# Optimization experiments

Hardware: AMD Instinct MI355X
Metric: run time of the kernel (lower is better)

Reference implementation:

```python
import jax, jax.numpy as jnp
import numpy as np

EPS = 1e-4   # synsin-style z clamp in world_to_view
BIG = 1e10   # z-buffer init


def _xy_grid(h, w):
    xs = jnp.linspace(-1.0, 1.0, w)
    ys = jnp.linspace(-1.0, 1.0, h)
    gy, gx = jnp.meshgrid(ys, xs, indexing='ij')
    return jnp.stack([gx.ravel(), gy.ravel()], 0)  # [2, h*w], NDC pixel rays


def _view_to_world(depth, K_inv, RTinv, xy):
    # depth [B,1,N]; homogeneous coords rows = (x*d, y*d, d, 1)
    proj = jnp.concatenate([xy[None] * depth, depth, jnp.ones_like(depth)], axis=1)  # [B,4,N]
    cam = jnp.einsum('bij,bjn->bin', K_inv, proj)
    return jnp.einsum('bij,bjn->bin', RTinv, cam)  # [B,4,N]


def _world_to_view(world, K, RT):
    cam2 = jnp.einsum('bij,bjn->bin', RT, world)
    xy_proj = jnp.einsum('bij,bjn->bin', K, cam2)
    z = xy_proj[:, 2:3]
    mask = jnp.abs(z) < EPS
    zs = jnp.where(mask, EPS, z)
    sampler = jnp.concatenate([xy_proj[:, 0:2] / zs, z], axis=1)  # [B,3,N]
    return jnp.where(mask, -10.0, sampler)


def _splat_one(sampler, feats, h, w):
    # sampler [3,N] (x,y in NDC, z depth); feats [C,N]. Nearest-pixel z-buffer splat.
    x, y, z = sampler[0], sampler[1], sampler[2]
    n = x.shape[0]
    px = jnp.round((x + 1.0) * 0.5 * (w - 1)).astype(jnp.int32)
    py = jnp.round((y + 1.0) * 0.5 * (h - 1)).astype(jnp.int32)
    valid = (px >= 0) & (px < w) & (py >= 0) & (py < h) & (z > EPS)
    idx = jnp.where(valid, py * w + px, h * w)  # invalid -> dump bucket h*w
    zv = jnp.where(valid, z, BIG)
    zbuf = jnp.full(h * w + 1, BIG, feats.dtype).at[idx].min(zv)
    pid = jnp.where(valid & (zv <= zbuf[idx]), jnp.arange(n, dtype=jnp.int32), n)
    win = jnp.full(h * w + 1, n, jnp.int32).at[idx].min(pid)[: h * w]  # winning point per pixel
    fpad = jnp.concatenate([feats, jnp.zeros((feats.shape[0], 1), feats.dtype)], axis=1)
    out = fpad[:, win].reshape(feats.shape[0], h, w)
    zb = zbuf[: h * w]
    depth = jnp.where(zb < BIG, zb, 0.0).reshape(1, h, w)
    return out, depth


def _project(depths, colors, feats, K, src_RTs, src_RTinvs, dst_RTs, dst_RTinvs):
    B, V, _, Hc, Wc = depths.shape
    _, _, C, Hf, Wf = feats.shape
    sh, sw = Hf / Hc, Wf / Wc
    scale = jnp.array([sw, sh, 1.0, 1.0], depths.dtype)[None, :, None]
    sK = K * scale
    sKinv = jnp.linalg.inv(sK)

    colors_r = jax.image.resize(colors.reshape(B * V, 3, Hc, Wc), (B * V, 3, Hf, Wf),
                                method='linear', antialias=True)
    depths_r = jax.image.resize(depths.reshape(B * V, 1, Hc, Wc), (B * V, 1, Hf, Wf),
                                method='nearest')
    feats_f = feats.reshape(B, V, C, Hf * Wf)
    colors_f = colors_r.reshape(B, V, 3, Hf * Wf)
    depths_f = depths_r.reshape(B, V, 1, Hf * Wf)

    xy = _xy_grid(Hf, Wf)
    dstRT = dst_RTs[:, 0]  # num_outputs == 1
    splat = jax.vmap(lambda s, f: _splat_one(s, f, Hf, Wf))

    results, warped, pdepths = [], [], []
    for i in range(V):  # small fixed number of source views
        world = _view_to_world(depths_f[:, i], sKinv, src_RTinvs[:, i], xy)
        sampler = _world_to_view(world, sK, dstRT)            # [B,3,N]
        src = jnp.concatenate([feats_f[:, i], colors_f[:, i] * 0.5 + 0.5], axis=1)  # [B,C+3,N]
        res, dep = splat(sampler, src)                        # [B,C+3,Hf,Wf], [B,1,Hf,Wf]
        results.append(res[:, :C])
        warped.append(res[:, C:])
        pdepths.append(dep)

    prj_fs = jnp.stack(results, 0)      # [V,B,C,Hf,Wf]
    warped = jnp.stack(warped, 0)       # [V,B,3,Hf,Wf]
    prj_depths = jnp.stack(pdepths, 0)  # [V,B,1,Hf,Wf]
    # forward() permutes prj_fs / prj_depths to [B,V,...]; warped stays [V,B,...]
    return prj_fs.transpose(1, 0, 2, 3, 4), warped, prj_depths.transpose(1, 0, 2, 3, 4)


def setup_inputs() -> dict:
    key = jax.random.key(0)
    k1, k2, k3 = jax.random.split(key, 3)
    B, V, Hc, Wc = 2, 2, 512, 512
    Hf, Wf, C = 256, 256, 64

    depths = jax.random.uniform(k1, (B, V, 1, Hc, Wc), jnp.float32, 1.0, 5.0)
    colors = jax.random.uniform(k2, (B, V, 3, Hc, Wc), jnp.float32, -1.0, 1.0)
    feats = jax.random.normal(k3, (B, V, C, Hf, Wf), jnp.float32)

    K = np.eye(4, dtype=np.float32)  # NDC intrinsic (fx=fy=1, cx=cy=0)
    th = 0.1
    R = np.array([[np.cos(th), 0, np.sin(th), 0.2],
                  [0, 1, 0, 0.0],
                  [-np.sin(th), 0, np.cos(th), 0.1],
                  [0, 0, 0, 1]], dtype=np.float32)
    src_RT = np.eye(4, dtype=np.float32)

    Kb = jnp.asarray(np.tile(K[None], (B, 1, 1)))
    src_RTs = jnp.asarray(np.tile(src_RT[None, None], (B, V, 1, 1)))
    src_RTinvs = src_RTs  # identity
    dst_RTs = jnp.asarray(np.tile(R[None, None], (B, 1, 1, 1)))
    dst_RTinvs = jnp.asarray(np.tile(np.linalg.inv(R)[None, None], (B, 1, 1, 1)))

    return {"depths": depths, "colors": colors, "feats": feats, "K": Kb,
            "src_RTs": src_RTs, "src_RTinvs": src_RTinvs,
            "dst_RTs": dst_RTs, "dst_RTinvs": dst_RTinvs}


def reference(depths, colors, feats, K, src_RTs, src_RTinvs, dst_RTs, dst_RTinvs):
    return _project(depths, colors, feats, K, src_RTs, src_RTinvs, dst_RTs, dst_RTinvs)
```

## Files before the change

kernel.cpp:

```cpp
#include <hip/hip_runtime.h>
#include <stdint.h>

#pragma clang fp contract(off)

namespace {
constexpr int B_ = 2, V_ = 2, HC = 512, WC = 512, HF = 256, WF = 256, CF = 64;
constexpr int NPIX = HF * WF;
constexpr float EPSF = 1e-4f;
constexpr float BIGF = 1e10f;
constexpr int NPT = B_ * V_ * NPIX;
constexpr int NBLK_PT = NPT / 256;
constexpr size_t WS_BASE = (size_t)NPT * 8 + (size_t)B_ * V_ * 3 * NPIX * 4 + 256;
constexpr size_t TF_BYTES = (size_t)NPT * CF * 4;
}

__device__ __forceinline__ float dot4f(const float* __restrict__ r,
                                       float v0, float v1, float v2, float v3) {
  float t = r[0] * v0;
  t = t + r[1] * v1;
  t = t + r[2] * v2;
  t = t + r[3] * v3;
  return t;
}

__global__ void prep_k(const float* __restrict__ K,
                       const float* __restrict__ colors,
                       float* __restrict__ colr,
                       float* __restrict__ mats,
                       unsigned long long* __restrict__ zwin) {
  int g = blockIdx.x * blockDim.x + threadIdx.x;

  if (g < NPT) zwin[g] = ~0ULL;

  if (g < B_) {
    int b = g;
    const float rowscale[4] = {0.5f, 0.5f, 1.0f, 1.0f};
    float sK[16];
    for (int i = 0; i < 4; ++i)
      for (int j = 0; j < 4; ++j)
        sK[i*4+j] = K[b*16 + i*4 + j] * rowscale[i];
    double m[16];
    for (int i = 0; i < 16; ++i) m[i] = (double)sK[i];
    double inv[16];
    inv[0]  =  m[5]*m[10]*m[15] - m[5]*m[11]*m[14] - m[9]*m[6]*m[15] + m[9]*m[7]*m[14] + m[13]*m[6]*m[11] - m[13]*m[7]*m[10];
    inv[4]  = -m[4]*m[10]*m[15] + m[4]*m[11]*m[14] + m[8]*m[6]*m[15] - m[8]*m[7]*m[14] - m[12]*m[6]*m[11] + m[12]*m[7]*m[10];
    inv[8]  =  m[4]*m[9]*m[15]  - m[4]*m[11]*m[13] - m[8]*m[5]*m[15] + m[8]*m[7]*m[13] + m[12]*m[5]*m[11] - m[12]*m[7]*m[9];
    inv[12] = -m[4]*m[9]*m[14]  + m[4]*m[10]*m[13] + m[8]*m[5]*m[14] - m[8]*m[6]*m[13] - m[12]*m[5]*m[10] + m[12]*m[6]*m[9];
    inv[1]  = -m[1]*m[10]*m[15] + m[1]*m[11]*m[14] + m[9]*m[2]*m[15] - m[9]*m[3]*m[14] - m[13]*m[2]*m[11] + m[13]*m[3]*m[10];
    inv[5]  =  m[0]*m[10]*m[15] - m[0]*m[11]*m[14] - m[8]*m[2]*m[15] + m[8]*m[3]*m[14] + m[12]*m[2]*m[11] - m[12]*m[3]*m[10];
    inv[9]  = -m[0]*m[9]*m[15]  + m[0]*m[11]*m[13] + m[8]*m[1]*m[15] - m[8]*m[3]*m[13] - m[12]*m[1]*m[11] + m[12]*m[3]*m[9];
    inv[13] =  m[0]*m[9]*m[14]  - m[0]*m[10]*m[13] - m[8]*m[1]*m[14] + m[8]*m[2]*m[13] + m[12]*m[1]*m[10] - m[12]*m[2]*m[9];
    inv[2]  =  m[1]*m[6]*m[15]  - m[1]*m[7]*m[14]  - m[5]*m[2]*m[15] + m[5]*m[3]*m[14] + m[13]*m[2]*m[7]  - m[13]*m[3]*m[6];
    inv[6]  = -m[0]*m[6]*m[15]  + m[0]*m[7]*m[14]  + m[4]*m[2]*m[15] - m[4]*m[3]*m[14] - m[12]*m[2]*m[7]  + m[12]*m[3]*m[6];
    inv[10] =  m[0]*m[5]*m[15]  - m[0]*m[7]*m[13]  - m[4]*m[1]*m[15] + m[4]*m[3]*m[13] + m[12]*m[1]*m[7]  - m[12]*m[3]*m[5];
    inv[14] = -m[0]*m[5]*m[14]  + m[0]*m[6]*m[13]  + m[4]*m[1]*m[14] - m[4]*m[2]*m[13] - m[12]*m[1]*m[6]  + m[12]*m[2]*m[5];
    inv[3]  = -m[1]*m[6]*m[11]  + m[1]*m[7]*m[10]  + m[5]*m[2]*m[11] - m[5]*m[3]*m[10] - m[9]*m[2]*m[7]   + m[9]*m[3]*m[6];
    inv[7]  =  m[0]*m[6]*m[11]  - m[0]*m[7]*m[10]  - m[4]*m[2]*m[11] + m[4]*m[3]*m[10] + m[8]*m[2]*m[7]   - m[8]*m[3]*m[6];
    inv[11] = -m[0]*m[5]*m[11]  + m[0]*m[7]*m[9]   + m[4]*m[1]*m[11] - m[4]*m[3]*m[9]  - m[8]*m[1]*m[7]   + m[8]*m[3]*m[5];
    inv[15] =  m[0]*m[5]*m[10]  - m[0]*m[6]*m[9]   - m[4]*m[1]*m[10] + m[4]*m[2]*m[9]  + m[8]*m[1]*m[6]   - m[8]*m[2]*m[5];
    double det = m[0]*inv[0] + m[1]*inv[4] + m[2]*inv[8] + m[3]*inv[12];
    double idet = 1.0 / det;
    for (int i = 0; i < 16; ++i) {
      mats[b*32 + i]      = sK[i];
      mats[b*32 + 16 + i] = (float)(inv[i] * idet);
    }
  }

  if (g >= B_ * V_ * 3 * NPIX) return;
  int pc  = g >> 16;
  int pix = g & (NPIX - 1);
  int y = pix >> 8, x = pix & (WF - 1);
  const float* src = colors + (size_t)pc * HC * WC;
  const float W37 = (float)(3.0 / 7.0), W17 = (float)(1.0 / 7.0);
  float wy[4] = {0.125f, 0.375f, 0.375f, 0.125f};
  float wx[4] = {0.125f, 0.375f, 0.375f, 0.125f};
  if (y == 0)      { wy[0] = 0.f; wy[1] = W37; wy[2] = W37; wy[3] = W17; }
  if (y == HF - 1) { wy[0] = W17; wy[1] = W37; wy[2] = W37; wy[3] = 0.f; }
  if (x == 0)      { wx[0] = 0.f; wx[1] = W37; wx[2] = W37; wx[3] = W17; }
  if (x == WF - 1) { wx[0] = W17; wx[1] = W37; wx[2] = W37; wx[3] = 0.f; }
  int jy0 = 2 * y - 1, jx0 = 2 * x - 1;
  float acc = 0.f;
  #pragma unroll
  for (int ty = 0; ty < 4; ++ty) {
    if (wy[ty] == 0.f) continue;
    int jy = jy0 + ty;
    float rs = 0.f;
    #pragma unroll
    for (int tx = 0; tx < 4; ++tx) {
      if (wx[tx] == 0.f) continue;
      rs = rs + wx[tx] * src[(size_t)jy * WC + (jx0 + tx)];
    }
    acc = acc + wy[ty] * rs;
  }
  colr[g] = acc;
}

__global__ void transp_k(const float* __restrict__ feats,
                         float* __restrict__ tf) {
  __shared__ float lds[CF][65];
  int bid = blockIdx.x;
  int bv = bid >> 10;
  int pix0 = (bid & 1023) << 6;
  int t = threadIdx.x;
  int sub = t >> 4;
  int l16 = t & 15;
  const float* fb = feats + (size_t)bv * CF * NPIX;
  #pragma unroll
  for (int pass = 0; pass < 4; ++pass) {
    int ch = pass * 16 + sub;
    const float4 v = *(const float4*)(fb + (size_t)ch * NPIX + pix0 + 4 * l16);
    lds[ch][4*l16+0] = v.x; lds[ch][4*l16+1] = v.y;
    lds[ch][4*l16+2] = v.z; lds[ch][4*l16+3] = v.w;
  }
  __syncthreads();
  float* tb = tf + ((size_t)bv * NPIX + pix0) * CF;
  #pragma unroll
  for (int pass = 0; pass < 4; ++pass) {
    int p = pass * 16 + sub;
    float4 w;
    w.x = lds[4*l16+0][p]; w.y = lds[4*l16+1][p];
    w.z = lds[4*l16+2][p]; w.w = lds[4*l16+3][p];
    *(float4*)(tb + (size_t)p * CF + 4 * l16) = w;
  }
}

__global__ void splat_k(const float* __restrict__ depths,
                        const float* __restrict__ mats,
                        const float* __restrict__ srcRTinv,
                        const float* __restrict__ dstRT,
                        unsigned long long* __restrict__ zwin) {
  int g = blockIdx.x * blockDim.x + threadIdx.x;
  if (g >= NPT) return;
  int bv = g >> 16;
  int n  = g & (NPIX - 1);
  int b  = bv / V_;
  int y = n >> 8, x = n & (WF - 1);
  float d = depths[(size_t)bv * HC * WC + (size_t)(2 * y + 1) * WC + (2 * x + 1)];
  const float step32 = 2.0f / 255.0f;
  float xf = (float)x * step32 - 1.0f;
  float yf = (float)y * step32 - 1.0f;
  float pr0 = xf * d, pr1 = yf * d, pr2 = d, pr3 = 1.0f;
  const float* sK  = mats + b * 32;
  const float* sKi = mats + b * 32 + 16;
  const float* Rs  = srcRTinv + (size_t)bv * 16;
  const float* Rd  = dstRT + (size_t)b * 16;
  float a0 = dot4f(sKi + 0,  pr0, pr1, pr2, pr3);
  float a1 = dot4f(sKi + 4,  pr0, pr1, pr2, pr3);
  float a2 = dot4f(sKi + 8,  pr0, pr1, pr2, pr3);
  float a3 = dot4f(sKi + 12, pr0, pr1, pr2, pr3);
  float w0 = dot4f(Rs + 0,  a0, a1, a2, a3);
  float w1 = dot4f(Rs + 4,  a0, a1, a2, a3);
  float w2 = dot4f(Rs + 8,  a0, a1, a2, a3);
  float w3 = dot4f(Rs + 12, a0, a1, a2, a3);
  float c0 = dot4f(Rd + 0,  w0, w1, w2, w3);
  float c1 = dot4f(Rd + 4,  w0, w1, w2, w3);
  float c2 = dot4f(Rd + 8,  w0, w1, w2, w3);
  float c3 = dot4f(Rd + 12, w0, w1, w2, w3);
  float p0 = dot4f(sK + 0, c0, c1, c2, c3);
  float p1 = dot4f(sK + 4, c0, c1, c2, c3);
  float p2 = dot4f(sK + 8, c0, c1, c2, c3);
  if (!(p2 > EPSF)) return;
  float sx = p0 / p2, sy = p1 / p2;
  float pxf = rintf(((sx + 1.0f) * 0.5f) * 255.0f);
  float pyf = rintf(((sy + 1.0f) * 0.5f) * 255.0f);
  if (!(pxf >= 0.0f && pxf <= 255.0f && pyf >= 0.0f && pyf <= 255.0f)) return;
  int idx = (int)pyf * WF + (int)pxf;
  unsigned zbits = __float_as_uint(p2);
  unsigned long long key = ((unsigned long long)zbits << 32) | (unsigned)n;
  atomicMin(&zwin[(size_t)bv * NPIX + idx], key);
}

__global__ void gatherT_k(const unsigned long long* __restrict__ zwin,
                          const float* __restrict__ tf,
                          const float* __restrict__ colr,
                          float* __restrict__ out0,
                          float* __restrict__ out1,
                          float* __restrict__ out2) {
  int g = blockIdx.x * 256 + threadIdx.x;
  int bv = g >> 16;
  int pix = g & (NPIX - 1);
  unsigned long long key = zwin[g];
  bool hit = (key != ~0ULL);
  int n = (int)(key & 0xffffffffULL);
  float4 f[16];
  if (hit) {
    const float4* src = (const float4*)(tf + ((size_t)bv * NPIX + n) * CF);
    #pragma unroll
    for (int i = 0; i < 16; ++i) f[i] = src[i];
  } else {
    #pragma unroll
    for (int i = 0; i < 16; ++i) f[i] = make_float4(0.f, 0.f, 0.f, 0.f);
  }
  float* o0 = out0 + (size_t)bv * CF * NPIX + pix;
  const float* fs = (const float*)f;
  #pragma unroll
  for (int c = 0; c < CF; ++c)
    __builtin_nontemporal_store(fs[c], &o0[(size_t)c * NPIX]);

  int b = bv >> 1, v = bv & 1;
  const float* cb = colr + (size_t)bv * 3 * NPIX;
  float* o1 = out1 + (size_t)(v * B_ + b) * 3 * NPIX + pix;
  if (hit) {
    float z = __uint_as_float((unsigned)(key >> 32));
    __builtin_nontemporal_store((z < BIGF) ? z : 0.0f, &out2[g]);
    #pragma unroll
    for (int ch = 0; ch < 3; ++ch)
      __builtin_nontemporal_store(cb[(size_t)ch * NPIX + n] * 0.5f + 0.5f,
                                  &o1[(size_t)ch * NPIX]);
  } else {
    __builtin_nontemporal_store(0.0f, &out2[g]);
    #pragma unroll
    for (int ch = 0; ch < 3; ++ch)
      __builtin_nontemporal_store(0.0f, &o1[(size_t)ch * NPIX]);
  }
}

__global__ void gather_k(const unsigned long long* __restrict__ zwin,
                         const float* __restrict__ feats,
                         const float* __restrict__ colr,
                         float* __restrict__ out0,
                         float* __restrict__ out1,
                         float* __restrict__ out2) {
  int bid = blockIdx.x;
  int grp = bid >> 10;
  int g   = (bid & (NBLK_PT - 1)) * 256 + threadIdx.x;
  int bv  = g >> 16;
  int pix = g & (NPIX - 1);
  unsigned long long key = zwin[g];
  bool hit = (key != ~0ULL);
  int n = (int)(key & 0xffffffffULL);

  if (grp < 4) {
    int c0 = grp * 16;
    const float* fb = feats + (size_t)bv * CF * NPIX + (size_t)c0 * NPIX;
    float* o0 = out0 + (size_t)bv * CF * NPIX + (size_t)c0 * NPIX + pix;
    if (hit) {
      #pragma unroll
      for (int c = 0; c < 16; ++c)
        __builtin_nontemporal_store(fb[(size_t)c * NPIX + n], &o0[(size_t)c * NPIX]);
    } else {
      #pragma unroll
      for (int c = 0; c < 16; ++c)
        __builtin_nontemporal_store(0.0f, &o0[(size_t)c * NPIX]);
    }
  } else {
    int b = bv >> 1, v = bv & 1;
    const float* cb = colr + (size_t)bv * 3 * NPIX;
    float* o1 = out1 + (size_t)(v * B_ + b) * 3 * NPIX + pix;
    if (hit) {
      float z = __uint_as_float((unsigned)(key >> 32));
      __builtin_nontemporal_store((z < BIGF) ? z : 0.0f, &out2[g]);
      #pragma unroll
      for (int ch = 0; ch < 3; ++ch)
        __builtin_nontemporal_store(cb[(size_t)ch * NPIX + n] * 0.5f + 0.5f,
                                    &o1[(size_t)ch * NPIX]);
    } else {
      __builtin_nontemporal_store(0.0f, &out2[g]);
      #pragma unroll
      for (int ch = 0; ch < 3; ++ch)
        __builtin_nontemporal_store(0.0f, &o1[(size_t)ch * NPIX]);
    }
  }
}

extern "C" void kernel_launch(void* const* d_in, const int* in_sizes, int n_in,
                              void* d_out, int out_size, void* d_ws, size_t ws_size,
                              hipStream_t stream) {
  const float* depths     = (const float*)d_in[0];
  const float* colors     = (const float*)d_in[1];
  const float* feats      = (const float*)d_in[2];
  const float* K          = (const float*)d_in[3];
  const float* src_RTinvs = (const float*)d_in[5];
  const float* dst_RTs    = (const float*)d_in[6];

  float* out0 = (float*)d_out;
  float* out1 = out0 + (size_t)B_ * V_ * CF * NPIX;
  float* out2 = out1 + (size_t)V_ * B_ * 3 * NPIX;

  unsigned long long* zwin = (unsigned long long*)d_ws;
  float* colr = (float*)(zwin + NPT);
  float* mats = colr + (size_t)B_ * V_ * 3 * NPIX;
  float* tf   = (float*)((char*)d_ws + WS_BASE);

  const bool use_tf = (ws_size >= WS_BASE + TF_BYTES);

  prep_k<<<(B_ * V_ * 3 * NPIX) / 256, 256, 0, stream>>>(K, colors, colr, mats, zwin);
  if (use_tf)
    transp_k<<<B_ * V_ * (NPIX / 64), 256, 0, stream>>>(feats, tf);
  splat_k<<<NBLK_PT, 256, 0, stream>>>(depths, mats, src_RTinvs, dst_RTs, zwin);
  if (use_tf)
    gatherT_k<<<NBLK_PT, 256, 0, stream>>>(zwin, tf, colr, out0, out1, out2);
  else
    gather_k<<<5 * NBLK_PT, 256, 0, stream>>>(zwin, feats, colr, out0, out1, out2);
}
```

Before: 184.7 us.

## Fuse feature transpose into prep kernel and split gather across channel groups

Moves the feature transpose into the prep kernel as extra blocks, which removes one kernel launch and lets transpose and colour resize run concurrently. Also splits the transposed gather kernel into five block groups: four each handle 16 feature channels and one handles colour and depth. This gives five times more blocks with fewer registers per thread, for more memory parallelism, at the cost of rereading zwin five times. The prep kernel now allocates LDS in every block, including the resize blocks that never use it, which may lower occupancy.

New measurement: 180.5 us. 2.3% less time.

```diff
diff --git a/kernel.cpp b/kernel.cpp
--- a/kernel.cpp
+++ b/kernel.cpp
@@ -10,6 +10,8 @@
 constexpr float BIGF = 1e10f;
 constexpr int NPT = B_ * V_ * NPIX;
 constexpr int NBLK_PT = NPT / 256;
+constexpr int RESIZE_BLKS = (B_ * V_ * 3 * NPIX) / 256;
+constexpr int TRANSP_BLKS = B_ * V_ * (NPIX / 64);
 constexpr size_t WS_BASE = (size_t)NPT * 8 + (size_t)B_ * V_ * 3 * NPIX * 4 + 256;
 constexpr size_t TF_BYTES = (size_t)NPT * CF * 4;
 }
@@ -25,10 +27,43 @@
 
 __global__ void prep_k(const float* __restrict__ K,
                        const float* __restrict__ colors,
+                       const float* __restrict__ feats,
                        float* __restrict__ colr,
                        float* __restrict__ mats,
-                       unsigned long long* __restrict__ zwin) {
-  int g = blockIdx.x * blockDim.x + threadIdx.x;
+                       unsigned long long* __restrict__ zwin,
+                       float* __restrict__ tf) {
+  __shared__ float lds[CF][65];
+  int bid = blockIdx.x;
+  int nT = (int)gridDim.x - RESIZE_BLKS;
+  int t = threadIdx.x;
+
+  if (bid < nT) {
+    int bv = bid >> 10;
+    int pix0 = (bid & 1023) << 6;
+    int sub = t >> 4;
+    int l16 = t & 15;
+    const float* fb = feats + (size_t)bv * CF * NPIX;
+    #pragma unroll
+    for (int pass = 0; pass < 4; ++pass) {
+      int ch = pass * 16 + sub;
+      const float4 v = *(const float4*)(fb + (size_t)ch * NPIX + pix0 + 4 * l16);
+      lds[ch][4*l16+0] = v.x; lds[ch][4*l16+1] = v.y;
+      lds[ch][4*l16+2] = v.z; lds[ch][4*l16+3] = v.w;
+    }
+    __syncthreads();
+    float* tb = tf + ((size_t)bv * NPIX + pix0) * CF;
+    #pragma unroll
+    for (int pass = 0; pass < 4; ++pass) {
+      int p = pass * 16 + sub;
+      float4 w;
+      w.x = lds[4*l16+0][p]; w.y = lds[4*l16+1][p];
+      w.z = lds[4*l16+2][p]; w.w = lds[4*l16+3][p];
+      *(float4*)(tb + (size_t)p * CF + 4 * l16) = w;
+    }
+    return;
+  }
+
+  int g = (bid - nT) * 256 + t;
 
   if (g < NPT) zwin[g] = ~0ULL;
 
@@ -66,7 +101,6 @@
     }
   }
 
-  if (g >= B_ * V_ * 3 * NPIX) return;
   int pc  = g >> 16;
   int pix = g & (NPIX - 1);
   int y = pix >> 8, x = pix & (WF - 1);
@@ -93,35 +127,6 @@
     acc = acc + wy[ty] * rs;
   }
   colr[g] = acc;
-}
-
-__global__ void transp_k(const float* __restrict__ feats,
-                         float* __restrict__ tf) {
-  __shared__ float lds[CF][65];
-  int bid = blockIdx.x;
-  int bv = bid >> 10;
-  int pix0 = (bid & 1023) << 6;
-  int t = threadIdx.x;
-  int sub = t >> 4;
-  int l16 = t & 15;
-  const float* fb = feats + (size_t)bv * CF * NPIX;
-  #pragma unroll
-  for (int pass = 0; pass < 4; ++pass) {
-    int ch = pass * 16 + sub;
-    const float4 v = *(const float4*)(fb + (size_t)ch * NPIX + pix0 + 4 * l16);
-    lds[ch][4*l16+0] = v.x; lds[ch][4*l16+1] = v.y;
-    lds[ch][4*l16+2] = v.z; lds[ch][4*l16+3] = v.w;
-  }
-  __syncthreads();
-  float* tb = tf + ((size_t)bv * NPIX + pix0) * CF;
-  #pragma unroll
-  for (int pass = 0; pass < 4; ++pass) {
-    int p = pass * 16 + sub;
-    float4 w;
-    w.x = lds[4*l16+0][p]; w.y = lds[4*l16+1][p];
-    w.z = lds[4*l16+2][p]; w.w = lds[4*l16+3][p];
-    *(float4*)(tb + (size_t)p * CF + 4 * l16) = w;
-  }
 }
 
 __global__ void splat_k(const float* __restrict__ depths,
@@ -176,42 +181,48 @@
                           float* __restrict__ out0,
                           float* __restrict__ out1,
                           float* __restrict__ out2) {
-  int g = blockIdx.x * 256 + threadIdx.x;
-  int bv = g >> 16;
+  int bid = blockIdx.x;
+  int grp = bid >> 10;
+  int g   = (bid & (NBLK_PT - 1)) * 256 + threadIdx.x;
+  int bv  = g >> 16;
   int pix = g & (NPIX - 1);
   unsigned long long key = zwin[g];
   bool hit = (key != ~0ULL);
   int n = (int)(key & 0xffffffffULL);
-  float4 f[16];
-  if (hit) {
-    const float4* src = (const float4*)(tf + ((size_t)bv * NPIX + n) * CF);
+
+  if (grp < 4) {
+    float4 f[4];
+    if (hit) {
+      const float4* src =
+          (const float4*)(tf + ((size_t)bv * NPIX + n) * CF + grp * 16);
+      #pragma unroll
+      for (int i = 0; i < 4; ++i) f[i] = src[i];
+    } else {
+      #pragma unroll
+      for (int i = 0; i < 4; ++i) f[i] = make_float4(0.f, 0.f, 0.f, 0.f);
+    }
+    float* o0 = out0 + (size_t)bv * CF * NPIX + (size_t)(grp * 16) * NPIX + pix;
+    const float* fs = (const float*)f;
     #pragma unroll
-    for (int i = 0; i < 16; ++i) f[i] = src[i];
+    for (int c = 0; c < 16; ++c)
+      __builtin_nontemporal_store(fs[c], &o0[(size_t)c * NPIX]);
   } else {
-    #pragma unroll
-    for (int i = 0; i < 16; ++i) f[i] = make_float4(0.f, 0.f, 0.f, 0.f);
-  }
-  float* o0 = out0 + (size_t)bv * CF * NPIX + pix;
-  const float* fs = (const float*)f;
-  #pragma unroll
-  for (int c = 0; c < CF; ++c)
-    __builtin_nontemporal_store(fs[c], &o0[(size_t)c * NPIX]);
-
-  int b = bv >> 1, v = bv & 1;
-  const float* cb = colr + (size_t)bv * 3 * NPIX;
-  float* o1 = out1 + (size_t)(v * B_ + b) * 3 * NPIX + pix;
-  if (hit) {
-    float z = __uint_as_float((unsigned)(key >> 32));
-    __builtin_nontemporal_store((z < BIGF) ? z : 0.0f, &out2[g]);
-    #pragma unroll
-    for (int ch = 0; ch < 3; ++ch)
-      __builtin_nontemporal_store(cb[(size_t)ch * NPIX + n] * 0.5f + 0.5f,
-                                  &o1[(size_t)ch * NPIX]);
-  } else {
-    __builtin_nontemporal_store(0.0f, &out2[g]);
-    #pragma unroll
-    for (int ch = 0; ch < 3; ++ch)
-      __builtin_nontemporal_store(0.0f, &o1[(size_t)ch * NPIX]);
+    int b = bv >> 1, v = bv & 1;
+    const float* cb = colr + (size_t)bv * 3 * NPIX;
+    float* o1 = out1 + (size_t)(v * B_ + b) * 3 * NPIX + pix;
+    if (hit) {
+      float z = __uint_as_float((unsigned)(key >> 32));
+      __builtin_nontemporal_store((z < BIGF) ? z : 0.0f, &out2[g]);
+      #pragma unroll
+      for (int ch = 0; ch < 3; ++ch)
+        __builtin_nontemporal_store(cb[(size_t)ch * NPIX + n] * 0.5f + 0.5f,
+                                    &o1[(size_t)ch * NPIX]);
+    } else {
+      __builtin_nontemporal_store(0.0f, &out2[g]);
+      #pragma unroll
+      for (int ch = 0; ch < 3; ++ch)
+        __builtin_nontemporal_store(0.0f, &o1[(size_t)ch * NPIX]);
+    }
   }
 }
 
@@ -284,12 +295,11 @@
 
   const bool use_tf = (ws_size >= WS_BASE + TF_BYTES);
 
-  prep_k<<<(B_ * V_ * 3 * NPIX) / 256, 256, 0, stream>>>(K, colors, colr, mats, zwin);
-  if (use_tf)
-    transp_k<<<B_ * V_ * (NPIX / 64), 256, 0, stream>>>(feats, tf);
+  int prep_grid = use_tf ? (TRANSP_BLKS + RESIZE_BLKS) : RESIZE_BLKS;
+  prep_k<<<prep_grid, 256, 0, stream>>>(K, colors, feats, colr, mats, zwin, tf);
   splat_k<<<NBLK_PT, 256, 0, stream>>>(depths, mats, src_RTinvs, dst_RTs, zwin);
   if (use_tf)
-    gatherT_k<<<NBLK_PT, 256, 0, stream>>>(zwin, tf, colr, out0, out1, out2);
+    gatherT_k<<<5 * NBLK_PT, 256, 0, stream>>>(zwin, tf, colr, out0, out1, out2);
   else
     gather_k<<<5 * NBLK_PT, 256, 0, stream>>>(zwin, feats, colr, out0, out1, out2);
 }
```
